# Kernel tuning notes

Measured on AMD Instinct MI355X. Metric: run time of the kernel, lower is better.

## Reference

```python
import jax, jax.numpy as jnp
import numpy as np

D_MODEL = 1024
NUM_HEAD = 16
D_K = D_MODEL // NUM_HEAD


def setup_inputs() -> dict:
    key = jax.random.key(0)
    ks = jax.random.split(key, 9)
    s = 1.0 / np.sqrt(D_MODEL)
    x = jax.random.normal(ks[0], (2, 2048, D_MODEL), dtype=jnp.float32)
    Wq = jax.random.uniform(ks[1], (D_MODEL, D_MODEL), jnp.float32, -s, s)
    bq = jax.random.uniform(ks[2], (D_MODEL,), jnp.float32, -s, s)
    Wk = jax.random.uniform(ks[3], (D_MODEL, D_MODEL), jnp.float32, -s, s)
    bk = jax.random.uniform(ks[4], (D_MODEL,), jnp.float32, -s, s)
    Wv = jax.random.uniform(ks[5], (D_MODEL, D_MODEL), jnp.float32, -s, s)
    bv = jax.random.uniform(ks[6], (D_MODEL,), jnp.float32, -s, s)
    Wo = jax.random.uniform(ks[7], (D_MODEL, D_MODEL), jnp.float32, -s, s)
    bo = jax.random.uniform(ks[8], (D_MODEL,), jnp.float32, -s, s)
    return {"x": x, "Wq": Wq, "bq": bq, "Wk": Wk, "bk": bk,
            "Wv": Wv, "bv": bv, "Wo": Wo, "bo": bo}


def reference(x, Wq, bq, Wk, bk, Wv, bv, Wo, bo):
    b, n, d = x.shape
    h, dk = NUM_HEAD, D_K
    # Linear projections (torch Linear: x @ W.T + b)
    q = (x @ Wq.T + bq).reshape(b, n, h, dk).transpose(0, 2, 1, 3)  # [b,h,n,dk]
    k = (x @ Wk.T + bk).reshape(b, n, h, dk).transpose(0, 2, 1, 3)
    v = (x @ Wv.T + bv).reshape(b, n, h, dk).transpose(0, 2, 1, 3)
    scores = jnp.einsum('bhqd,bhkd->bhqk', q, k) / jnp.sqrt(jnp.float32(dk))
    attn = jax.nn.softmax(scores, axis=-1)  # [b,h,n,n]
    out = jnp.einsum('bhqk,bhkd->bhqd', attn, v)
    out = out.transpose(0, 2, 1, 3).reshape(b, n, d)
    return out @ Wo.T + bo
```

## Files before the change

### kernel.cpp

```cpp
#include <hip/hip_runtime.h>

#define BATCH   2
#define SEQ     2048
#define DMODEL  1024
#define NHEAD   16
#define DKH     64
#define MTOT    (BATCH*SEQ)
#define KDIM    DMODEL

#define XB    0u
#define WQB   (4u*1024u*1024u)
#define WKB   (5u*1024u*1024u)
#define WVB   (6u*1024u*1024u)
#define WOB   (7u*1024u*1024u)
#define QOFF  (8u*1024u*1024u)
#define KOFF  (12u*1024u*1024u)
#define VOFF  (16u*1024u*1024u)
#define OOFF  (20u*1024u*1024u)

typedef __bf16 bf16x8 __attribute__((ext_vector_type(8)));
typedef __bf16 bf16x4 __attribute__((ext_vector_type(4)));
typedef float  f32x4  __attribute__((ext_vector_type(4)));
typedef float  f32x16 __attribute__((ext_vector_type(16)));

__device__ __forceinline__ void async16(const __bf16* g, __bf16* l) {
  __builtin_amdgcn_global_load_lds(
      (const __attribute__((address_space(1))) void*)g,
      (__attribute__((address_space(3))) void*)l, 16, 0, 0);
}

__device__ __forceinline__ unsigned cvtpk_bf16(float lo, float hi) {
  unsigned r;
  asm("v_cvt_pk_bf16_f32 %0, %1, %2" : "=v"(r) : "v"(lo), "v"(hi));
  return r;
}
__device__ __forceinline__ void plswap(unsigned& a, unsigned& b) {
  asm("v_permlane32_swap_b32 %0, %1" : "+v"(a), "+v"(b));
}

__global__ __launch_bounds__(256) void cvt_fp32_bf16(
    const float* __restrict__ x,  const float* __restrict__ wq,
    const float* __restrict__ wk, const float* __restrict__ wv,
    const float* __restrict__ wo, __bf16* __restrict__ ws)
{
  const float* src; __bf16* dst; int n;
  switch (blockIdx.y) {
    case 0:  src = x;  dst = ws + XB;  n = 4 * 1024 * 1024; break;
    case 1:  src = wq; dst = ws + WQB; n = 1024 * 1024;     break;
    case 2:  src = wk; dst = ws + WKB; n = 1024 * 1024;     break;
    case 3:  src = wv; dst = ws + WVB; n = 1024 * 1024;     break;
    default: src = wo; dst = ws + WOB; n = 1024 * 1024;     break;
  }
  const int i = (blockIdx.x * 256 + threadIdx.x) * 8;
  if (i < n) {
    const float4 a = *(const float4*)(src + i);
    const float4 b = *(const float4*)(src + i + 4);
    bf16x8 o;
    o[0] = (__bf16)a.x; o[1] = (__bf16)a.y; o[2] = (__bf16)a.z; o[3] = (__bf16)a.w;
    o[4] = (__bf16)b.x; o[5] = (__bf16)b.y; o[6] = (__bf16)b.z; o[7] = (__bf16)b.w;
    *(bf16x8*)(dst + i) = o;
  }
}

__device__ __forceinline__ void gemm128_core(
    const __bf16* __restrict__ A, const __bf16* __restrict__ W,
    int m0, int n0, __bf16* lds, f32x4 (&acc)[4][4])
{
  __bf16* A_lds = lds;
  __bf16* B_lds = lds + 4096;
  const int t    = threadIdx.x;
  const int w    = t >> 6;
  const int lane = t & 63;
  const int ln15 = lane & 15;
  const int quad = lane >> 4;
  const int wr   = (w >> 1) << 6;
  const int wc   = (w & 1) << 6;

#pragma unroll
  for (int i = 0; i < 4; ++i)
#pragma unroll
    for (int j = 0; j < 4; ++j) acc[i][j] = (f32x4){0.f, 0.f, 0.f, 0.f};

  for (int kt = 0; kt < KDIM; kt += 32) {
    __syncthreads();
#pragma unroll
    for (int issue = 0; issue < 2; ++issue) {
      const int cbase = issue * 256 + (w << 6);
      const int c     = cbase + lane;
      const int row   = c >> 2;
      const int goff  = ((c & 3) ^ (row & 3)) << 3;
      async16(A + (size_t)(m0 + row) * KDIM + kt + goff, A_lds + cbase * 8);
      async16(W + (size_t)(n0 + row) * KDIM + kt + goff, B_lds + cbase * 8);
    }
    __syncthreads();

    bf16x8 af[4], bfr[4];
#pragma unroll
    for (int i = 0; i < 4; ++i) {
      const int row = wr + i * 16 + ln15;
      af[i] = *(const bf16x8*)&A_lds[row * 32 + ((quad ^ (row & 3)) << 3)];
    }
#pragma unroll
    for (int j = 0; j < 4; ++j) {
      const int row = wc + j * 16 + ln15;
      bfr[j] = *(const bf16x8*)&B_lds[row * 32 + ((quad ^ (row & 3)) << 3)];
    }
#pragma unroll
    for (int i = 0; i < 4; ++i)
#pragma unroll
      for (int j = 0; j < 4; ++j)
        acc[i][j] = __builtin_amdgcn_mfma_f32_16x16x32_bf16(af[i], bfr[j], acc[i][j], 0, 0, 0);
  }
}

__global__ __launch_bounds__(256) void qkv_gemm(
    const __bf16* __restrict__ X,
    const __bf16* __restrict__ Wq, const float* __restrict__ bq,
    const __bf16* __restrict__ Wk, const float* __restrict__ bk,
    const __bf16* __restrict__ Wv, const float* __restrict__ bv,
    __bf16* __restrict__ ws)
{
  __shared__ __align__(16) __bf16 lds[128 * 64];

  const int z = blockIdx.z;
  const __bf16* W    = (z == 0) ? Wq : (z == 1) ? Wk : Wv;
  const float*  bias = (z == 0) ? bq : (z == 1) ? bk : bv;
  __bf16* out = ws + ((z == 0) ? QOFF : (z == 1) ? KOFF : VOFF);
  const float scale = (z == 0) ? 0.125f * 1.44269504088896f : 1.0f;

  const int m0 = blockIdx.x * 128;
  const int n0 = blockIdx.y * 128;

  f32x4 acc[4][4];
  gemm128_core(X, W, m0, n0, lds, acc);

  const int t = threadIdx.x, w = t >> 6, lane = t & 63;
  const int ln15 = lane & 15, quad = lane >> 4;
  const int wr = (w >> 1) << 6, wc = (w & 1) << 6;

  float bj4[4];
#pragma unroll
  for (int j = 0; j < 4; ++j) bj4[j] = bias[n0 + wc + j * 16 + ln15];

  __syncthreads();
  __bf16* scr = lds + (w << 10);

  const int bb = m0 >> 11;
  const int s_base = (m0 & 2047) + wr;
  const int h = (n0 + wc) >> 6;

  if (z != 2) {
    const int rdrow = lane & 15, rdseg = lane >> 4;
#pragma unroll
    for (int i = 0; i < 4; ++i) {
#pragma unroll
      for (int j = 0; j < 4; ++j)
#pragma unroll
        for (int rr = 0; rr < 4; ++rr)
          scr[(quad * 4 + rr) * 64 + j * 16 + ln15] =
              (__bf16)((acc[i][j][rr] + bj4[j]) * scale);
      bf16x8 v0 = *(const bf16x8*)&scr[rdrow * 64 + rdseg * 16];
      bf16x8 v1 = *(const bf16x8*)&scr[rdrow * 64 + rdseg * 16 + 8];
      const int s = s_base + i * 16 + rdrow;
      __bf16* p = out + (((size_t)(bb * NHEAD + h)) * SEQ + s) * DKH + rdseg * 16;
      *(bf16x8*)p = v0;
      *(bf16x8*)&p[8] = v1;
    }
  } else {
#pragma unroll
    for (int i = 0; i < 4; ++i) {
#pragma unroll
      for (int j = 0; j < 4; ++j) {
        bf16x4 pk;
#pragma unroll
        for (int rr = 0; rr < 4; ++rr) pk[rr] = (__bf16)(acc[i][j][rr] + bj4[j]);
        *(bf16x4*)&scr[(j * 16 + ln15) * 16 + quad * 4] = pk;
      }
      bf16x8 c0 = *(const bf16x8*)&scr[lane * 16];
      bf16x8 c1 = *(const bf16x8*)&scr[lane * 16 + 8];
      __bf16* p = out + (((size_t)(bb * NHEAD + h)) * DKH + lane) * SEQ
                      + s_base + i * 16;
      *(bf16x8*)p = c0;
      *(bf16x8*)&p[8] = c1;
    }
  }
}

__global__ __launch_bounds__(256) void out_gemm(
    const __bf16* __restrict__ A, const __bf16* __restrict__ Wo,
    const float* __restrict__ bo, float* __restrict__ out)
{
  __shared__ __align__(16) __bf16 lds[6144];
  __bf16* A_lds = lds;
  __bf16* B_lds = lds + 2048;

  const int m0 = blockIdx.x * 64;
  const int n0 = blockIdx.y * 128;

  const int t = threadIdx.x, w = t >> 6, lane = t & 63;
  const int ln15 = lane & 15, quad = lane >> 4;

  f32x4 acc[4][2];
#pragma unroll
  for (int i = 0; i < 4; ++i)
#pragma unroll
    for (int j = 0; j < 2; ++j) acc[i][j] = (f32x4){0.f, 0.f, 0.f, 0.f};

  for (int kt = 0; kt < KDIM; kt += 32) {
    __syncthreads();
    {
      const int c = (w << 6) + lane;
      const int row = c >> 2;
      const int goff = ((c & 3) ^ (row & 3)) << 3;
      async16(A + (size_t)(m0 + row) * KDIM + kt + goff, A_lds + c * 8);
    }
#pragma unroll
    for (int issue = 0; issue < 2; ++issue) {
      const int cbase = issue * 256 + (w << 6);
      const int c = cbase + lane;
      const int row = c >> 2;
      const int goff = ((c & 3) ^ (row & 3)) << 3;
      async16(Wo + (size_t)(n0 + row) * KDIM + kt + goff, B_lds + cbase * 8);
    }
    __syncthreads();

    bf16x8 af[4], bfr[2];
#pragma unroll
    for (int i = 0; i < 4; ++i) {
      const int row = i * 16 + ln15;
      af[i] = *(const bf16x8*)&A_lds[row * 32 + ((quad ^ (row & 3)) << 3)];
    }
#pragma unroll
    for (int j = 0; j < 2; ++j) {
      const int row = (w << 5) + j * 16 + ln15;
      bfr[j] = *(const bf16x8*)&B_lds[row * 32 + ((quad ^ (row & 3)) << 3)];
    }
#pragma unroll
    for (int i = 0; i < 4; ++i)
#pragma unroll
      for (int j = 0; j < 2; ++j)
        acc[i][j] = __builtin_amdgcn_mfma_f32_16x16x32_bf16(af[i], bfr[j], acc[i][j], 0, 0, 0);
  }

  float bj2[2];
#pragma unroll
  for (int j = 0; j < 2; ++j) bj2[j] = bo[n0 + (w << 5) + j * 16 + ln15];

  __syncthreads();
  float* scrf = (float*)lds + (w << 9);

  const int rdrow = lane & 15, rdseg = lane >> 4;
#pragma unroll
  for (int i = 0; i < 4; ++i) {
#pragma unroll
    for (int j = 0; j < 2; ++j) {
      f32x4 v;
#pragma unroll
      for (int rr = 0; rr < 4; ++rr) v[rr] = acc[i][j][rr] + bj2[j];
      *(f32x4*)&scrf[(j * 16 + ln15) * 16 + quad * 4] = v;
    }
    const int m = m0 + i * 16 + rdrow;
    float* p = out + (size_t)m * DMODEL + n0 + (w << 5) + rdseg * 8;
#pragma unroll
    for (int cc = 0; cc < 2; ++cc) {
      f32x4 v;
#pragma unroll
      for (int e = 0; e < 4; ++e)
        v[e] = scrf[(rdseg * 8 + cc * 4 + e) * 16 + rdrow];
      *(f32x4*)&p[cc * 4] = v;
    }
  }
}

__device__ __forceinline__ void softmax_frag(const f32x16& s, float& l,
                                             bf16x8& pfa, bf16x8& pfb)
{
  float p[16];
#pragma unroll
  for (int r = 0; r < 16; ++r) {
    p[r] = __builtin_amdgcn_exp2f(s[r]);
    l += p[r];
  }
  unsigned A0 = cvtpk_bf16(p[0],  p[1]);
  unsigned A1 = cvtpk_bf16(p[2],  p[3]);
  unsigned B0 = cvtpk_bf16(p[4],  p[5]);
  unsigned B1 = cvtpk_bf16(p[6],  p[7]);
  unsigned C0 = cvtpk_bf16(p[8],  p[9]);
  unsigned C1 = cvtpk_bf16(p[10], p[11]);
  unsigned D0 = cvtpk_bf16(p[12], p[13]);
  unsigned D1 = cvtpk_bf16(p[14], p[15]);
  plswap(A0, B0);
  plswap(A1, B1);
  plswap(C0, D0);
  plswap(C1, D1);
  union { unsigned u[4]; bf16x8 v; } ua, ub;
  ua.u[0] = A0; ua.u[1] = A1; ua.u[2] = B0; ua.u[3] = B1;
  ub.u[0] = C0; ub.u[1] = C1; ub.u[2] = D0; ub.u[3] = D1;
  pfa = ua.v;
  pfb = ub.v;
}

__device__ __forceinline__ void pvstep(const __bf16* Vs, int kh, int KS, int hl,
                                       int ln31, const bf16x8& PF,
                                       f32x16& o0, f32x16& o1)
{
  const int vchunk = (kh << 3) + 2 * KS + hl;
  bf16x8 vf0 = *(const bf16x8*)&Vs[ln31 * 128 + ((vchunk ^ (ln31 & 15)) << 3)];
  bf16x8 vf1 = *(const bf16x8*)&Vs[(32 + ln31) * 128 +
                                   ((vchunk ^ ((32 + ln31) & 15)) << 3)];
  o0 = __builtin_amdgcn_mfma_f32_32x32x16_bf16(PF, vf0, o0, 0, 0, 0);
  o1 = __builtin_amdgcn_mfma_f32_32x32x16_bf16(PF, vf1, o1, 0, 0, 0);
}

__device__ __forceinline__ void attn_tile_compute(
    const __bf16* Ks, const __bf16* Vs, const bf16x8 (&qf)[4],
    int kh, int ln31, int hl, float& l_lane, f32x16& o0, f32x16& o1)
{
#pragma unroll
  for (int half = 0; half < 2; ++half) {
    f32x16 s;
#pragma unroll
    for (int r = 0; r < 16; ++r) s[r] = 0.f;
    const int kr = (kh << 6) + half * 32 + ln31;
    __builtin_amdgcn_s_setprio(1);
#pragma unroll
    for (int ks = 0; ks < 4; ++ks) {
      bf16x8 kf = *(const bf16x8*)&Ks[kr * 64 + (((2 * ks + hl) ^ (kr & 7)) << 3)];
      s = __builtin_amdgcn_mfma_f32_32x32x16_bf16(kf, qf[ks], s, 0, 0, 0);
    }
    __builtin_amdgcn_s_setprio(0);
    bf16x8 pa, pb;
    softmax_frag(s, l_lane, pa, pb);
    __builtin_amdgcn_s_setprio(1);
    pvstep(Vs, kh, half * 2 + 0, hl, ln31, pa, o0, o1);
    pvstep(Vs, kh, half * 2 + 1, hl, ln31, pb, o0, o1);
    __builtin_amdgcn_s_setprio(0);
  }
}

__global__ __launch_bounds__(512, 4) void attn_kernel(
    const __bf16* __restrict__ Qb, const __bf16* __restrict__ Kb,
    const __bf16* __restrict__ Vtb, __bf16* __restrict__ Ob)
{
  __shared__ __align__(16) __bf16 smem[5 * 128 * 64];
  __bf16* QP = smem;
  __bf16* Ks = smem + 8192;
  __bf16* Vs = smem + 24576;

  const int t = threadIdx.x, w = t >> 6, lane = t & 63;
  const int ln31 = lane & 31, hl = lane >> 5;
  const int g  = w & 3;
  const int kh = w >> 2;
  const int bh = blockIdx.x;
  const int q0 = blockIdx.y * 128;
  const int bb = bh >> 4, hh = bh & 15;

  const __bf16* Qg = Qb + (size_t)bh * SEQ * DKH + (size_t)q0 * DKH;
  const __bf16* Kg = Kb + (size_t)bh * SEQ * DKH;
  const __bf16* Vg = Vtb + (size_t)bh * DKH * SEQ;

#pragma unroll
  for (int issue = 0; issue < 2; ++issue) {
    const int cbase = issue * 512 + (w << 6);
    const int c = cbase + lane;
    const int row = c >> 3;
    const int goff = ((c & 7) ^ (row & 7)) << 3;
    async16(Qg + (size_t)row * DKH + goff, QP + cbase * 8);
  }
  __syncthreads();

  const int qrow = (g << 5) + ln31;
  bf16x8 qf[4];
#pragma unroll
  for (int ks = 0; ks < 4; ++ks) {
    const int chunk = ((2 * ks + hl) ^ (qrow & 7));
    qf[ks] = *(const bf16x8*)&QP[qrow * 64 + (chunk << 3)];
  }

  float l_lane = 0.f;
  f32x16 o0, o1;
#pragma unroll
  for (int r = 0; r < 16; ++r) { o0[r] = 0.f; o1[r] = 0.f; }

  for (int kt = 0; kt < SEQ; kt += 256) {
    __syncthreads();
#pragma unroll
    for (int sub = 0; sub < 2; ++sub) {
      __bf16* Kd = Ks + sub * 8192;
      __bf16* Vd = Vs + sub * 8192;
      const int ktе_base = kt + sub * 128;
#pragma unroll
      for (int issue = 0; issue < 2; ++issue) {
        const int cbase = issue * 512 + (w << 6);
        const int c = cbase + lane;
        const int krow = c >> 3;
        const int kgoff = ((c & 7) ^ (krow & 7)) << 3;
        async16(Kg + (size_t)(ktе_base + krow) * DKH + kgoff, Kd + cbase * 8);
        const int vrow = c >> 4;
        const int vgoff = ((c & 15) ^ (vrow & 15)) << 3;
        async16(Vg + (size_t)vrow * SEQ + ktе_base + vgoff, Vd + cbase * 8);
      }
    }
    __syncthreads();

    attn_tile_compute(Ks,        Vs,        qf, kh, ln31, hl, l_lane, o0, o1);
    attn_tile_compute(Ks + 8192, Vs + 8192, qf, kh, ln31, hl, l_lane, o0, o1);
  }

  __syncthreads();
  float* cmb = (float*)smem;
  const int dsw = ln31 & 7;
  l_lane += __shfl_xor(l_lane, 32);

  if (w >= 4) {
    float* base = cmb + (g << 11);
#pragma unroll
    for (int gg = 0; gg < 4; ++gg) {
      const int qq = ((2 * gg + hl) ^ dsw) << 2;
      f32x4 va, vb;
#pragma unroll
      for (int rr = 0; rr < 4; ++rr) { va[rr] = o0[4 * gg + rr]; vb[rr] = o1[4 * gg + rr]; }
      *(f32x4*)&base[ln31 * 32 + qq]        = va;
      *(f32x4*)&base[(32 + ln31) * 32 + qq] = vb;
    }
    if (hl == 0) cmb[8192 + (g << 5) + ln31] = l_lane;
  }
  __syncthreads();
  if (w < 4) {
    float* base = cmb + (g << 11);
#pragma unroll
    for (int gg = 0; gg < 4; ++gg) {
      const int qq = ((2 * gg + hl) ^ dsw) << 2;
      const f32x4 va = *(const f32x4*)&base[ln31 * 32 + qq];
      const f32x4 vb = *(const f32x4*)&base[(32 + ln31) * 32 + qq];
#pragma unroll
      for (int rr = 0; rr < 4; ++rr) { o0[4 * gg + rr] += va[rr]; o1[4 * gg + rr] += vb[rr]; }
    }
    const float inv = 1.0f / (l_lane + cmb[8192 + (g << 5) + ln31]);

#pragma unroll
    for (int r = 0; r < 16; ++r) {
      const int qi = (r & 3) + 8 * (r >> 2) + 4 * hl;
      const float iq = __shfl(inv, qi);
      const int q = q0 + (g << 5) + qi;
      __bf16* rowp = Ob + ((size_t)(bb * SEQ + q)) * DMODEL + hh * DKH;
      rowp[ln31]      = (__bf16)(o0[r] * iq);
      rowp[32 + ln31] = (__bf16)(o1[r] * iq);
    }
  }
}

extern "C" void kernel_launch(void* const* d_in, const int* in_sizes, int n_in,
                              void* d_out, int out_size, void* d_ws, size_t ws_size,
                              hipStream_t stream)
{
  const float* x  = (const float*)d_in[0];
  const float* Wq = (const float*)d_in[1];
  const float* bq = (const float*)d_in[2];
  const float* Wk = (const float*)d_in[3];
  const float* bk = (const float*)d_in[4];
  const float* Wv = (const float*)d_in[5];
  const float* bv = (const float*)d_in[6];
  const float* Wo = (const float*)d_in[7];
  const float* bo = (const float*)d_in[8];
  float*  out = (float*)d_out;
  __bf16* ws  = (__bf16*)d_ws;

  cvt_fp32_bf16<<<dim3(2048, 5, 1), 256, 0, stream>>>(x, Wq, Wk, Wv, Wo, ws);

  qkv_gemm<<<dim3(MTOT / 128, DMODEL / 128, 3), 256, 0, stream>>>(
      ws + XB, ws + WQB, bq, ws + WKB, bk, ws + WVB, bv, ws);

  attn_kernel<<<dim3(BATCH * NHEAD, SEQ / 128), 512, 0, stream>>>(
      ws + QOFF, ws + KOFF, ws + VOFF, ws + OOFF);

  out_gemm<<<dim3(MTOT / 64, DMODEL / 128), 256, 0, stream>>>(
      ws + OOFF, ws + WOB, bo, out);
}
```

Baseline: 186.4 us.

## Split attention keys four ways across 16 waves with 1024-thread blocks

The attention kernel moves from 8 waves (2 key-halves × 4 query groups) to 16 waves (4 key-quarters × 4 query groups) per block. Each iteration now loads a single 128-key K/V tile instead of two, which shrinks shared memory to 3 tiles. Partial outputs are combined by a serial three-step shared-memory reduction into the first wave group. This raises wave-level parallelism per block, at the cost of twice as many barrier-separated tile loads, a longer reduction, and tighter register limits from the new launch bounds.

```diff
diff --git a/kernel.cpp b/kernel.cpp
--- a/kernel.cpp
+++ b/kernel.cpp
@@ -300,11 +300,11 @@
   pfb = ub.v;
 }
 
-__device__ __forceinline__ void pvstep(const __bf16* Vs, int kh, int KS, int hl,
+__device__ __forceinline__ void pvstep(const __bf16* Vs, int kq, int KS, int hl,
                                        int ln31, const bf16x8& PF,
                                        f32x16& o0, f32x16& o1)
 {
-  const int vchunk = (kh << 3) + 2 * KS + hl;
+  const int vchunk = (kq << 2) + 2 * KS + hl;
   bf16x8 vf0 = *(const bf16x8*)&Vs[ln31 * 128 + ((vchunk ^ (ln31 & 15)) << 3)];
   bf16x8 vf1 = *(const bf16x8*)&Vs[(32 + ln31) * 128 +
                                    ((vchunk ^ ((32 + ln31) & 15)) << 3)];
@@ -312,16 +312,65 @@
   o1 = __builtin_amdgcn_mfma_f32_32x32x16_bf16(PF, vf1, o1, 0, 0, 0);
 }
 
-__device__ __forceinline__ void attn_tile_compute(
-    const __bf16* Ks, const __bf16* Vs, const bf16x8 (&qf)[4],
-    int kh, int ln31, int hl, float& l_lane, f32x16& o0, f32x16& o1)
-{
-#pragma unroll
-  for (int half = 0; half < 2; ++half) {
+__global__ __launch_bounds__(1024, 8) void attn_kernel(
+    const __bf16* __restrict__ Qb, const __bf16* __restrict__ Kb,
+    const __bf16* __restrict__ Vtb, __bf16* __restrict__ Ob)
+{
+  __shared__ __align__(16) __bf16 smem[3 * 128 * 64];
+  __bf16* QP = smem;
+  __bf16* Ks = smem + 8192;
+  __bf16* Vs = smem + 16384;
+
+  const int t = threadIdx.x, w = t >> 6, lane = t & 63;
+  const int ln31 = lane & 31, hl = lane >> 5;
+  const int qg = w & 3;
+  const int kq = w >> 2;
+  const int bh = blockIdx.x;
+  const int q0 = blockIdx.y * 128;
+  const int bb = bh >> 4, hh = bh & 15;
+
+  const __bf16* Qg = Qb + (size_t)bh * SEQ * DKH + (size_t)q0 * DKH;
+  const __bf16* Kg = Kb + (size_t)bh * SEQ * DKH;
+  const __bf16* Vg = Vtb + (size_t)bh * DKH * SEQ;
+
+  {
+    const int c = t;
+    const int row = c >> 3;
+    const int goff = ((c & 7) ^ (row & 7)) << 3;
+    async16(Qg + (size_t)row * DKH + goff, QP + c * 8);
+  }
+  __syncthreads();
+
+  const int qrow = (qg << 5) + ln31;
+  bf16x8 qf[4];
+#pragma unroll
+  for (int ks = 0; ks < 4; ++ks) {
+    const int chunk = ((2 * ks + hl) ^ (qrow & 7));
+    qf[ks] = *(const bf16x8*)&QP[qrow * 64 + (chunk << 3)];
+  }
+
+  float l_lane = 0.f;
+  f32x16 o0, o1;
+#pragma unroll
+  for (int r = 0; r < 16; ++r) { o0[r] = 0.f; o1[r] = 0.f; }
+
+  for (int kt = 0; kt < SEQ; kt += 128) {
+    __syncthreads();
+    {
+      const int c = t;
+      const int krow = c >> 3;
+      const int kgoff = ((c & 7) ^ (krow & 7)) << 3;
+      async16(Kg + (size_t)(kt + krow) * DKH + kgoff, Ks + c * 8);
+      const int vrow = c >> 4;
+      const int vgoff = ((c & 15) ^ (vrow & 15)) << 3;
+      async16(Vg + (size_t)vrow * SEQ + kt + vgoff, Vs + c * 8);
+    }
+    __syncthreads();
+
     f32x16 s;
 #pragma unroll
     for (int r = 0; r < 16; ++r) s[r] = 0.f;
-    const int kr = (kh << 6) + half * 32 + ln31;
+    const int kr = (kq << 5) + ln31;
     __builtin_amdgcn_s_setprio(1);
 #pragma unroll
     for (int ks = 0; ks < 4; ++ks) {
@@ -332,79 +381,9 @@
     bf16x8 pa, pb;
     softmax_frag(s, l_lane, pa, pb);
     __builtin_amdgcn_s_setprio(1);
-    pvstep(Vs, kh, half * 2 + 0, hl, ln31, pa, o0, o1);
-    pvstep(Vs, kh, half * 2 + 1, hl, ln31, pb, o0, o1);
+    pvstep(Vs, kq, 0, hl, ln31, pa, o0, o1);
+    pvstep(Vs, kq, 1, hl, ln31, pb, o0, o1);
     __builtin_amdgcn_s_setprio(0);
-  }
-}
-
-__global__ __launch_bounds__(512, 4) void attn_kernel(
-    const __bf16* __restrict__ Qb, const __bf16* __restrict__ Kb,
-    const __bf16* __restrict__ Vtb, __bf16* __restrict__ Ob)
-{
-  __shared__ __align__(16) __bf16 smem[5 * 128 * 64];
-  __bf16* QP = smem;
-  __bf16* Ks = smem + 8192;
-  __bf16* Vs = smem + 24576;
-
-  const int t = threadIdx.x, w = t >> 6, lane = t & 63;
-  const int ln31 = lane & 31, hl = lane >> 5;
-  const int g  = w & 3;
-  const int kh = w >> 2;
-  const int bh = blockIdx.x;
-  const int q0 = blockIdx.y * 128;
-  const int bb = bh >> 4, hh = bh & 15;
-
-  const __bf16* Qg = Qb + (size_t)bh * SEQ * DKH + (size_t)q0 * DKH;
-  const __bf16* Kg = Kb + (size_t)bh * SEQ * DKH;
-  const __bf16* Vg = Vtb + (size_t)bh * DKH * SEQ;
-
-#pragma unroll
-  for (int issue = 0; issue < 2; ++issue) {
-    const int cbase = issue * 512 + (w << 6);
-    const int c = cbase + lane;
-    const int row = c >> 3;
-    const int goff = ((c & 7) ^ (row & 7)) << 3;
-    async16(Qg + (size_t)row * DKH + goff, QP + cbase * 8);
-  }
-  __syncthreads();
-
-  const int qrow = (g << 5) + ln31;
-  bf16x8 qf[4];
-#pragma unroll
-  for (int ks = 0; ks < 4; ++ks) {
-    const int chunk = ((2 * ks + hl) ^ (qrow & 7));
-    qf[ks] = *(const bf16x8*)&QP[qrow * 64 + (chunk << 3)];
-  }
-
-  float l_lane = 0.f;
-  f32x16 o0, o1;
-#pragma unroll
-  for (int r = 0; r < 16; ++r) { o0[r] = 0.f; o1[r] = 0.f; }
-
-  for (int kt = 0; kt < SEQ; kt += 256) {
-    __syncthreads();
-#pragma unroll
-    for (int sub = 0; sub < 2; ++sub) {
-      __bf16* Kd = Ks + sub * 8192;
-      __bf16* Vd = Vs + sub * 8192;
-      const int ktе_base = kt + sub * 128;
-#pragma unroll
-      for (int issue = 0; issue < 2; ++issue) {
-        const int cbase = issue * 512 + (w << 6);
-        const int c = cbase + lane;
-        const int krow = c >> 3;
-        const int kgoff = ((c & 7) ^ (krow & 7)) << 3;
-        async16(Kg + (size_t)(ktе_base + krow) * DKH + kgoff, Kd + cbase * 8);
-        const int vrow = c >> 4;
-        const int vgoff = ((c & 15) ^ (vrow & 15)) << 3;
-        async16(Vg + (size_t)vrow * SEQ + ktе_base + vgoff, Vd + cbase * 8);
-      }
-    }
-    __syncthreads();
-
-    attn_tile_compute(Ks,        Vs,        qf, kh, ln31, hl, l_lane, o0, o1);
-    attn_tile_compute(Ks + 8192, Vs + 8192, qf, kh, ln31, hl, l_lane, o0, o1);
   }
 
   __syncthreads();
@@ -412,37 +391,45 @@
   const int dsw = ln31 & 7;
   l_lane += __shfl_xor(l_lane, 32);
 
-  if (w >= 4) {
-    float* base = cmb + (g << 11);
-#pragma unroll
-    for (int gg = 0; gg < 4; ++gg) {
-      const int qq = ((2 * gg + hl) ^ dsw) << 2;
-      f32x4 va, vb;
-#pragma unroll
-      for (int rr = 0; rr < 4; ++rr) { va[rr] = o0[4 * gg + rr]; vb[rr] = o1[4 * gg + rr]; }
-      *(f32x4*)&base[ln31 * 32 + qq]        = va;
-      *(f32x4*)&base[(32 + ln31) * 32 + qq] = vb;
-    }
-    if (hl == 0) cmb[8192 + (g << 5) + ln31] = l_lane;
-  }
-  __syncthreads();
-  if (w < 4) {
-    float* base = cmb + (g << 11);
-#pragma unroll
-    for (int gg = 0; gg < 4; ++gg) {
-      const int qq = ((2 * gg + hl) ^ dsw) << 2;
-      const f32x4 va = *(const f32x4*)&base[ln31 * 32 + qq];
-      const f32x4 vb = *(const f32x4*)&base[(32 + ln31) * 32 + qq];
-#pragma unroll
-      for (int rr = 0; rr < 4; ++rr) { o0[4 * gg + rr] += va[rr]; o1[4 * gg + rr] += vb[rr]; }
-    }
-    const float inv = 1.0f / (l_lane + cmb[8192 + (g << 5) + ln31]);
+#pragma unroll
+  for (int r = 1; r < 4; ++r) {
+    if (kq == r) {
+      float* base = cmb + (qg << 11);
+#pragma unroll
+      for (int gg = 0; gg < 4; ++gg) {
+        const int qq = ((2 * gg + hl) ^ dsw) << 2;
+        f32x4 va, vb;
+#pragma unroll
+        for (int rr = 0; rr < 4; ++rr) { va[rr] = o0[4 * gg + rr]; vb[rr] = o1[4 * gg + rr]; }
+        *(f32x4*)&base[ln31 * 32 + qq]        = va;
+        *(f32x4*)&base[(32 + ln31) * 32 + qq] = vb;
+      }
+      if (hl == 0) cmb[8192 + (qg << 5) + ln31] = l_lane;
+    }
+    __syncthreads();
+    if (kq == 0) {
+      float* base = cmb + (qg << 11);
+#pragma unroll
+      for (int gg = 0; gg < 4; ++gg) {
+        const int qq = ((2 * gg + hl) ^ dsw) << 2;
+        const f32x4 va = *(const f32x4*)&base[ln31 * 32 + qq];
+        const f32x4 vb = *(const f32x4*)&base[(32 + ln31) * 32 + qq];
+#pragma unroll
+        for (int rr = 0; rr < 4; ++rr) { o0[4 * gg + rr] += va[rr]; o1[4 * gg + rr] += vb[rr]; }
+      }
+      l_lane += cmb[8192 + (qg << 5) + ln31];
+    }
+    __syncthreads();
+  }
+
+  if (kq == 0) {
+    const float inv = 1.0f / l_lane;
 
 #pragma unroll
     for (int r = 0; r < 16; ++r) {
       const int qi = (r & 3) + 8 * (r >> 2) + 4 * hl;
       const float iq = __shfl(inv, qi);
-      const int q = q0 + (g << 5) + qi;
+      const int q = q0 + (qg << 5) + qi;
       __bf16* rowp = Ob + ((size_t)(bb * SEQ + q)) * DMODEL + hh * DKH;
       rowp[ln31]      = (__bf16)(o0[r] * iq);
       rowp[32 + ln31] = (__bf16)(o1[r] * iq);
@@ -471,7 +458,7 @@
   qkv_gemm<<<dim3(MTOT / 128, DMODEL / 128, 3), 256, 0, stream>>>(
       ws + XB, ws + WQB, bq, ws + WKB, bk, ws + WVB, bv, ws);
 
-  attn_kernel<<<dim3(BATCH * NHEAD, SEQ / 128), 512, 0, stream>>>(
+  attn_kernel<<<dim3(BATCH * NHEAD, SEQ / 128), 1024, 0, stream>>>(
       ws + QOFF, ws + KOFF, ws + VOFF, ws + OOFF);
 
   out_gemm<<<dim3(MTOT / 64, DMODEL / 128), 256, 0, stream>>>(
```

Measured after the change: 264.5 us. 41.9% more time.

## Prefetch K/V tiles through registers and shrink attention LDS footprint

Applied to the files above, without the earlier changes.

Replaces the async global-to-LDS loads of two 128-key K/V tiles per iteration with register prefetching. The next 128-key tile is loaded into registers while the current tile is computed, then written to LDS at the top of the next iteration. This shrinks shared memory from five to three 16 KB tiles, and the launch-bounds occupancy hint drops from 4 to 2. The aim is to overlap global load latency with MFMA work, at the cost of more VGPRs, twice as many barrier pairs per key sweep, and a lower occupancy target.

```diff
diff --git a/kernel.cpp b/kernel.cpp
--- a/kernel.cpp
+++ b/kernel.cpp
@@ -338,14 +338,14 @@
   }
 }
 
-__global__ __launch_bounds__(512, 4) void attn_kernel(
+__global__ __launch_bounds__(512, 2) void attn_kernel(
     const __bf16* __restrict__ Qb, const __bf16* __restrict__ Kb,
     const __bf16* __restrict__ Vtb, __bf16* __restrict__ Ob)
 {
-  __shared__ __align__(16) __bf16 smem[5 * 128 * 64];
+  __shared__ __align__(16) __bf16 smem[3 * 128 * 64];
   __bf16* QP = smem;
   __bf16* Ks = smem + 8192;
-  __bf16* Vs = smem + 24576;
+  __bf16* Vs = smem + 16384;
 
   const int t = threadIdx.x, w = t >> 6, lane = t & 63;
   const int ln31 = lane & 31, hl = lane >> 5;
@@ -367,6 +367,24 @@
     const int goff = ((c & 7) ^ (row & 7)) << 3;
     async16(Qg + (size_t)row * DKH + goff, QP + cbase * 8);
   }
+
+  const int c0 = t, c1 = t + 512;
+  const int krow0 = c0 >> 3; const int kgo0 = ((c0 & 7) ^ (krow0 & 7)) << 3;
+  const int krow1 = c1 >> 3; const int kgo1 = ((c1 & 7) ^ (krow1 & 7)) << 3;
+  const int vrow0 = c0 >> 4; const int vgo0 = ((c0 & 15) ^ (vrow0 & 15)) << 3;
+  const int vrow1 = c1 >> 4; const int vgo1 = ((c1 & 15) ^ (vrow1 & 15)) << 3;
+  const __bf16* kp0 = Kg + (size_t)krow0 * DKH + kgo0;
+  const __bf16* kp1 = Kg + (size_t)krow1 * DKH + kgo1;
+  const __bf16* vp0 = Vg + (size_t)vrow0 * SEQ + vgo0;
+  const __bf16* vp1 = Vg + (size_t)vrow1 * SEQ + vgo1;
+  __bf16* kd0 = Ks + c0 * 8;  __bf16* kd1 = Ks + c1 * 8;
+  __bf16* vd0 = Vs + c0 * 8;  __bf16* vd1 = Vs + c1 * 8;
+
+  bf16x8 krg0 = *(const bf16x8*)kp0;
+  bf16x8 krg1 = *(const bf16x8*)kp1;
+  bf16x8 vrg0 = *(const bf16x8*)vp0;
+  bf16x8 vrg1 = *(const bf16x8*)vp1;
+
   __syncthreads();
 
   const int qrow = (g << 5) + ln31;
@@ -382,29 +400,18 @@
 #pragma unroll
   for (int r = 0; r < 16; ++r) { o0[r] = 0.f; o1[r] = 0.f; }
 
-  for (int kt = 0; kt < SEQ; kt += 256) {
-    __syncthreads();
-#pragma unroll
-    for (int sub = 0; sub < 2; ++sub) {
-      __bf16* Kd = Ks + sub * 8192;
-      __bf16* Vd = Vs + sub * 8192;
-      const int ktе_base = kt + sub * 128;
-#pragma unroll
-      for (int issue = 0; issue < 2; ++issue) {
-        const int cbase = issue * 512 + (w << 6);
-        const int c = cbase + lane;
-        const int krow = c >> 3;
-        const int kgoff = ((c & 7) ^ (krow & 7)) << 3;
-        async16(Kg + (size_t)(ktе_base + krow) * DKH + kgoff, Kd + cbase * 8);
-        const int vrow = c >> 4;
-        const int vgoff = ((c & 15) ^ (vrow & 15)) << 3;
-        async16(Vg + (size_t)vrow * SEQ + ktе_base + vgoff, Vd + cbase * 8);
-      }
-    }
-    __syncthreads();
-
-    attn_tile_compute(Ks,        Vs,        qf, kh, ln31, hl, l_lane, o0, o1);
-    attn_tile_compute(Ks + 8192, Vs + 8192, qf, kh, ln31, hl, l_lane, o0, o1);
+  for (int kt = 0; kt < SEQ; kt += 128) {
+    __syncthreads();
+    *(bf16x8*)kd0 = krg0;  *(bf16x8*)kd1 = krg1;
+    *(bf16x8*)vd0 = vrg0;  *(bf16x8*)vd1 = vrg1;
+    __syncthreads();
+    if (kt + 128 < SEQ) {
+      krg0 = *(const bf16x8*)(kp0 + (size_t)(kt + 128) * DKH);
+      krg1 = *(const bf16x8*)(kp1 + (size_t)(kt + 128) * DKH);
+      vrg0 = *(const bf16x8*)(vp0 + kt + 128);
+      vrg1 = *(const bf16x8*)(vp1 + kt + 128);
+    }
+    attn_tile_compute(Ks, Vs, qf, kh, ln31, hl, l_lane, o0, o1);
   }
 
   __syncthreads();
```

Measured after the change: 187.1 us. Within noise of the previous version (+0.4%).
